# Kernel optimization log

Hardware: AMD Instinct MI355X
Metric: run time of the kernel (lower is better)

The kernel has to match this reference:

```python
import jax, jax.numpy as jnp
import numpy as np
from jax import lax

RSM_K = 35
PFM_K = 31


def _box_sum(x, k):
    # Separable zero-padded box sum, equivalent to conv2d with a uniform kxk
    # kernel and padding=k//2 (odd k -> SAME). x: [B,1,H,W]
    p = k // 2
    pad = ((0, 0), (0, 0), (p, p), (0, 0))
    x = lax.reduce_window(x, 0.0, lax.add, (1, 1, k, 1), (1, 1, 1, 1), pad)
    pad = ((0, 0), (0, 0), (0, 0), (p, p))
    x = lax.reduce_window(x, 0.0, lax.add, (1, 1, 1, k), (1, 1, 1, 1), pad)
    return x


def _dilate(x, k):
    # Separable morphological dilation == max_pool2d(kernel=k, stride=1, pad=k//2).
    # -inf padding matches torch's max_pool2d padding semantics for 0/1 masks.
    p = k // 2
    ninf = -jnp.inf
    pad = ((0, 0), (0, 0), (p, p), (0, 0))
    x = lax.reduce_window(x, ninf, lax.max, (1, 1, k, 1), (1, 1, 1, 1), pad)
    pad = ((0, 0), (0, 0), (0, 0), (p, p))
    x = lax.reduce_window(x, ninf, lax.max, (1, 1, 1, k), (1, 1, 1, 1), pad)
    return x


def setup_inputs() -> dict:
    key = jax.random.key(0)
    # Sparse binary lesion mask, values exactly 0.0 / 1.0, shape [B,1,H,W]
    masks = (jax.random.uniform(key, (32, 1, 768, 768)) < 0.02).astype(jnp.float32)
    return {"masks": masks}


def reference(masks):
    # RSM: probability map = uniform 35x35 box average (conv2d with 1/k^2 kernel)
    rsm = _box_sum(masks, RSM_K) * (1.0 / (RSM_K * RSM_K))  # [B,1,H,W]
    # PFM: 1 = lesion, 0 = surrounding (inside 31x31 dilation), 2 = ignore
    dilated = _dilate(masks, PFM_K)
    pfm = jnp.where(masks > 0.5, 1, jnp.where(dilated > 0.5, 0, 2))
    pfm = pfm.astype(jnp.int32)[:, 0, :, :]  # [B,H,W]
    return rsm, pfm
```

## Files before the change

kernel.cpp:

```cpp
#include <hip/hip_runtime.h>


#define BATCH 32
#define HH 768
#define WW 768
#define NPIX (HH * WW)

constexpr int TYO  = 48;
constexpr int HALO = 17;
constexpr int ROWS = TYO + 2 * HALO;
constexpr int NSEG = 12;
constexpr int SSEG = NSEG + 2;
constexpr int NT   = 768;
constexpr int NG   = 4;
constexpr int RPG  = TYO / NG;
constexpr int CT   = 192;
constexpr int CPT  = 4;

__global__ __launch_bounds__(NT)
void label_gen_fused(const float* __restrict__ in, float* __restrict__ out) {
    __shared__ unsigned long long sbits[ROWS][SSEG];

    const int tid  = threadIdx.x;
    const int lane = tid & 63;
    const int wv   = tid >> 6;
    const int y0   = blockIdx.x * TYO;
    const int b    = blockIdx.y;
    const float* __restrict__ src = in + (size_t)b * NPIX;

    for (int lr = wv; lr < ROWS; lr += 12) {
        const int r = y0 - HALO + lr;
        unsigned long long bb[NSEG];
        if ((unsigned)r < (unsigned)HH) {
            const float* rp = src + (size_t)r * WW;
            #pragma unroll
            for (int j = 0; j < NSEG; ++j)
                bb[j] = __ballot(rp[64 * j + lane] > 0.5f);
        } else {
            #pragma unroll
            for (int j = 0; j < NSEG; ++j) bb[j] = 0ull;
        }
        if (lane == 0) {
            sbits[lr][0] = 0ull;
            #pragma unroll
            for (int j = 0; j < NSEG; ++j) sbits[lr][j + 1] = bb[j];
            sbits[lr][SSEG - 1] = 0ull;
        }
    }
    __syncthreads();

    const int g   = tid / CT;
    const int ct  = tid - g * CT;
    const int c0  = CPT * ct;
    const int yb  = y0 + RPG * g;
    const int lr0 = RPG * g;
    const int s   = c0 - HALO;
    const int q   = (s >> 6) + 1;
    const int sh  = s & 63;

    auto win = [&](int lr) -> unsigned long long {
        return (sbits[lr][q] >> sh) | (sbits[lr][q + 1] << (64 - sh));
    };
    const unsigned long long M35 = (1ull << 35) - 1;
    const unsigned long long M31 = (1ull << 31) - 1;
    auto bit = [](unsigned long long w, int k) -> int { return (int)((w >> k) & 1ull); };

    auto h35swar = [&](unsigned long long w) -> uint2 {
        const int h0 = (int)__popcll(w & M35);
        const int h1 = h0 + bit(w, 35) - bit(w, 0);
        const int h2 = h1 + bit(w, 36) - bit(w, 1);
        const int h3 = h2 + bit(w, 37) - bit(w, 2);
        return make_uint2((unsigned)(h0 | (h1 << 16)), (unsigned)(h2 | (h3 << 16)));
    };
    auto h31swar = [&](unsigned long long w) -> uint2 {
        const int d0 = (int)__popcll((w >> 2) & M31);
        const int d1 = d0 + bit(w, 33) - bit(w, 2);
        const int d2 = d1 + bit(w, 34) - bit(w, 3);
        const int d3 = d2 + bit(w, 35) - bit(w, 4);
        return make_uint2((unsigned)(d0 | (d1 << 16)), (unsigned)(d2 | (d3 << 16)));
    };

    uint2 v35 = make_uint2(0u, 0u), v31 = make_uint2(0u, 0u);
    #pragma unroll
    for (int k = 0; k < 35; ++k) {
        const unsigned long long w = win(lr0 + k);
        const uint2 a = h35swar(w);
        v35.x += a.x; v35.y += a.y;
        if (k >= 2 && k <= 32) {
            const uint2 d = h31swar(w);
            v31.x += d.x; v31.y += d.y;
        }
    }

    float* orow = out + (size_t)b * NPIX + (size_t)yb * WW + c0;
    float* prow = orow + (size_t)BATCH * NPIX;

    for (int i = 0; i < RPG; ++i) {
        const int lr = lr0 + HALO + i;
        const unsigned long long mwin = win(lr);

        float4 r4, p4;
        r4.x = (float)(v35.x & 0xFFFFu) * (1.0f / 1225.0f);
        r4.y = (float)(v35.x >> 16)     * (1.0f / 1225.0f);
        r4.z = (float)(v35.y & 0xFFFFu) * (1.0f / 1225.0f);
        r4.w = (float)(v35.y >> 16)     * (1.0f / 1225.0f);
        p4.x = bit(mwin, 17) ? 1.0f : ((v31.x & 0xFFFFu) ? 0.0f : 2.0f);
        p4.y = bit(mwin, 18) ? 1.0f : ((v31.x >> 16)     ? 0.0f : 2.0f);
        p4.z = bit(mwin, 19) ? 1.0f : ((v31.y & 0xFFFFu) ? 0.0f : 2.0f);
        p4.w = bit(mwin, 20) ? 1.0f : ((v31.y >> 16)     ? 0.0f : 2.0f);

        *(float4*)orow = r4;
        *(float4*)prow = p4;
        orow += WW; prow += WW;

        if (i < RPG - 1) {
            const uint2 e35 = h35swar(win(lr + 18));
            const uint2 l35 = h35swar(win(lr - 17));
            const uint2 e31 = h31swar(win(lr + 16));
            const uint2 l31 = h31swar(win(lr - 15));
            v35.x = v35.x + e35.x - l35.x;  v35.y = v35.y + e35.y - l35.y;
            v31.x = v31.x + e31.x - l31.x;  v31.y = v31.y + e31.y - l31.y;
        }
    }
}

extern "C" void kernel_launch(void* const* d_in, const int* in_sizes, int n_in,
                              void* d_out, int out_size, void* d_ws, size_t ws_size,
                              hipStream_t stream) {
    const float* masks = (const float*)d_in[0];
    float* out = (float*)d_out;
    dim3 grid(HH / TYO, BATCH);
    label_gen_fused<<<grid, NT, 0, stream>>>(masks, out);
}
```

Measured before the change: 213.9 us.

## Precompute per-row packed horizontal sums in LDS to share across vertical windows

```diff
diff --git a/kernel.cpp b/kernel.cpp
--- a/kernel.cpp
+++ b/kernel.cpp
@@ -15,11 +15,11 @@
 constexpr int NG   = 4;
 constexpr int RPG  = TYO / NG;
 constexpr int CT   = 192;
-constexpr int CPT  = 4;
 
 __global__ __launch_bounds__(NT)
 void label_gen_fused(const float* __restrict__ in, float* __restrict__ out) {
     __shared__ unsigned long long sbits[ROWS][SSEG];
+    __shared__ unsigned int hm[ROWS][CT];
 
     const int tid  = threadIdx.x;
     const int lane = tid & 63;
@@ -28,7 +28,7 @@
     const int b    = blockIdx.y;
     const float* __restrict__ src = in + (size_t)b * NPIX;
 
-    for (int lr = wv; lr < ROWS; lr += 12) {
+    for (int lr = wv; lr < ROWS; lr += NT / 64) {
         const int r = y0 - HALO + lr;
         unsigned long long bb[NSEG];
         if ((unsigned)r < (unsigned)HH) {
@@ -49,47 +49,57 @@
     }
     __syncthreads();
 
+    {
+        const int r0 = tid / CT;
+        const int ct = tid - r0 * CT;
+        const int c0 = 4 * ct;
+        const int s  = c0 - HALO;
+        const int q  = (s >> 6) + 1;
+        const int sh = s & 63;
+        const unsigned long long M35 = (1ull << 35) - 1;
+        for (int lr = r0; lr < ROWS; lr += NG) {
+            const unsigned long long w =
+                (sbits[lr][q] >> sh) | (sbits[lr][q + 1] << (64 - sh));
+            const int h0 = (int)__popcll(w & M35);
+            const int h1 = h0 + (int)((w >> 35) & 1) - (int)(w & 1);
+            const int h2 = h1 + (int)((w >> 36) & 1) - (int)((w >> 1) & 1);
+            const int h3 = h2 + (int)((w >> 37) & 1) - (int)((w >> 2) & 1);
+            unsigned long long sm = w | (w >> 1);
+            sm |= sm >> 2; sm |= sm >> 4; sm |= sm >> 8;
+            const unsigned int o4 = (unsigned int)(((sm >> 2) | (sm >> 17)) & 0xFull);
+            const unsigned int m4 = (unsigned int)((w >> 17) & 0xFull);
+            const unsigned int mb =
+                (((m4 & 1u) | ((m4 & 2u) << 7) | ((m4 & 4u) << 14) | ((m4 & 8u) << 21)) << 6);
+            const unsigned int ob =
+                (((o4 & 1u) | ((o4 & 2u) << 7) | ((o4 & 4u) << 14) | ((o4 & 8u) << 21)) << 7);
+            hm[lr][ct] = (unsigned)h0 | ((unsigned)h1 << 8) | ((unsigned)h2 << 16)
+                       | ((unsigned)h3 << 24) | mb | ob;
+        }
+    }
+    __syncthreads();
+
     const int g   = tid / CT;
     const int ct  = tid - g * CT;
-    const int c0  = CPT * ct;
+    const int c0  = 4 * ct;
     const int yb  = y0 + RPG * g;
     const int lr0 = RPG * g;
-    const int s   = c0 - HALO;
-    const int q   = (s >> 6) + 1;
-    const int sh  = s & 63;
 
-    auto win = [&](int lr) -> unsigned long long {
-        return (sbits[lr][q] >> sh) | (sbits[lr][q + 1] << (64 - sh));
-    };
-    const unsigned long long M35 = (1ull << 35) - 1;
-    const unsigned long long M31 = (1ull << 31) - 1;
-    auto bit = [](unsigned long long w, int k) -> int { return (int)((w >> k) & 1ull); };
+    const unsigned int M6 = 0x003F003Fu;
+    const unsigned int M1 = 0x01010101u;
 
-    auto h35swar = [&](unsigned long long w) -> uint2 {
-        const int h0 = (int)__popcll(w & M35);
-        const int h1 = h0 + bit(w, 35) - bit(w, 0);
-        const int h2 = h1 + bit(w, 36) - bit(w, 1);
-        const int h3 = h2 + bit(w, 37) - bit(w, 2);
-        return make_uint2((unsigned)(h0 | (h1 << 16)), (unsigned)(h2 | (h3 << 16)));
-    };
-    auto h31swar = [&](unsigned long long w) -> uint2 {
-        const int d0 = (int)__popcll((w >> 2) & M31);
-        const int d1 = d0 + bit(w, 33) - bit(w, 2);
-        const int d2 = d1 + bit(w, 34) - bit(w, 3);
-        const int d3 = d2 + bit(w, 35) - bit(w, 4);
-        return make_uint2((unsigned)(d0 | (d1 << 16)), (unsigned)(d2 | (d3 << 16)));
-    };
-
-    uint2 v35 = make_uint2(0u, 0u), v31 = make_uint2(0u, 0u);
+    unsigned int vA = 0, vB = 0;
+    unsigned int c31 = 0;
+    unsigned int ring_e[2], ring_l[2];
     #pragma unroll
     for (int k = 0; k < 35; ++k) {
-        const unsigned long long w = win(lr0 + k);
-        const uint2 a = h35swar(w);
-        v35.x += a.x; v35.y += a.y;
-        if (k >= 2 && k <= 32) {
-            const uint2 d = h31swar(w);
-            v31.x += d.x; v31.y += d.y;
-        }
+        const unsigned int x = hm[lr0 + k][ct];
+        vA += x & M6;
+        vB += (x >> 8) & M6;
+        if (k >= 2 && k <= 32) c31 += (x >> 7) & M1;
+        if (k == 0)  ring_l[0] = x;
+        if (k == 1)  ring_l[1] = x;
+        if (k == 33) ring_e[0] = x;
+        if (k == 34) ring_e[1] = x;
     }
 
     float* orow = out + (size_t)b * NPIX + (size_t)yb * WW + c0;
@@ -97,29 +107,32 @@
 
     for (int i = 0; i < RPG; ++i) {
         const int lr = lr0 + HALO + i;
-        const unsigned long long mwin = win(lr);
+        const unsigned int xc = hm[lr][ct];
 
         float4 r4, p4;
-        r4.x = (float)(v35.x & 0xFFFFu) * (1.0f / 1225.0f);
-        r4.y = (float)(v35.x >> 16)     * (1.0f / 1225.0f);
-        r4.z = (float)(v35.y & 0xFFFFu) * (1.0f / 1225.0f);
-        r4.w = (float)(v35.y >> 16)     * (1.0f / 1225.0f);
-        p4.x = bit(mwin, 17) ? 1.0f : ((v31.x & 0xFFFFu) ? 0.0f : 2.0f);
-        p4.y = bit(mwin, 18) ? 1.0f : ((v31.x >> 16)     ? 0.0f : 2.0f);
-        p4.z = bit(mwin, 19) ? 1.0f : ((v31.y & 0xFFFFu) ? 0.0f : 2.0f);
-        p4.w = bit(mwin, 20) ? 1.0f : ((v31.y >> 16)     ? 0.0f : 2.0f);
+        r4.x = (float)(vA & 0xFFFFu) * (1.0f / 1225.0f);
+        r4.y = (float)(vB & 0xFFFFu) * (1.0f / 1225.0f);
+        r4.z = (float)(vA >> 16)     * (1.0f / 1225.0f);
+        r4.w = (float)(vB >> 16)     * (1.0f / 1225.0f);
+        p4.x = ((xc >> 6) & 1u)  ? 1.0f : ((c31 & 0xFFu)         ? 0.0f : 2.0f);
+        p4.y = ((xc >> 14) & 1u) ? 1.0f : (((c31 >> 8) & 0xFFu)  ? 0.0f : 2.0f);
+        p4.z = ((xc >> 22) & 1u) ? 1.0f : (((c31 >> 16) & 0xFFu) ? 0.0f : 2.0f);
+        p4.w = ((xc >> 30) & 1u) ? 1.0f : ((c31 >> 24)           ? 0.0f : 2.0f);
 
         *(float4*)orow = r4;
         *(float4*)prow = p4;
         orow += WW; prow += WW;
 
         if (i < RPG - 1) {
-            const uint2 e35 = h35swar(win(lr + 18));
-            const uint2 l35 = h35swar(win(lr - 17));
-            const uint2 e31 = h31swar(win(lr + 16));
-            const uint2 l31 = h31swar(win(lr - 15));
-            v35.x = v35.x + e35.x - l35.x;  v35.y = v35.y + e35.y - l35.y;
-            v31.x = v31.x + e31.x - l31.x;  v31.y = v31.y + e31.y - l31.y;
+            const unsigned int xe   = hm[lr + 18][ct];
+            const unsigned int xl31 = hm[lr0 + 2 + i][ct];
+            const unsigned int xe31 = ring_e[i & 1];
+            const unsigned int xl   = ring_l[i & 1];
+            ring_e[i & 1] = xe;
+            ring_l[i & 1] = xl31;
+            vA  = (vA + (xe & M6)) - (xl & M6);
+            vB  = (vB + ((xe >> 8) & M6)) - ((xl >> 8) & M6);
+            c31 = (c31 + ((xe31 >> 7) & M1)) - ((xl31 >> 7) & M1);
         }
     }
 }
```

Measured after the change: 211.8 us. Within noise of the previous version (-1.0%).

## Precompute packed horizontal sums into LDS ring and roll vertical window per column

Applied to the files above, without the earlier changes.

```diff
diff --git a/kernel.cpp b/kernel.cpp
--- a/kernel.cpp
+++ b/kernel.cpp
@@ -7,19 +7,19 @@
 #define NPIX (HH * WW)
 
 constexpr int TYO  = 48;
-constexpr int HALO = 17;
-constexpr int ROWS = TYO + 2 * HALO;
 constexpr int NSEG = 12;
 constexpr int SSEG = NSEG + 2;
 constexpr int NT   = 768;
-constexpr int NG   = 4;
-constexpr int RPG  = TYO / NG;
 constexpr int CT   = 192;
-constexpr int CPT  = 4;
+constexpr int PRO  = 34;
+constexpr int RING = 48;
+
+__device__ __forceinline__ int m48(int x) { return (x >= RING) ? x - RING : x; }
 
 __global__ __launch_bounds__(NT)
-void label_gen_fused(const float* __restrict__ in, float* __restrict__ out) {
-    __shared__ unsigned long long sbits[ROWS][SSEG];
+void label_gen_roll(const float* __restrict__ in, float* __restrict__ out) {
+    __shared__ unsigned long long sbits[PRO][SSEG];
+    __shared__ unsigned int hm[RING][CT];
 
     const int tid  = threadIdx.x;
     const int lane = tid & 63;
@@ -28,8 +28,8 @@
     const int b    = blockIdx.y;
     const float* __restrict__ src = in + (size_t)b * NPIX;
 
-    for (int lr = wv; lr < ROWS; lr += 12) {
-        const int r = y0 - HALO + lr;
+    auto packrow = [&](int lr, int slot) {
+        const int r = y0 - 17 + lr;
         unsigned long long bb[NSEG];
         if ((unsigned)r < (unsigned)HH) {
             const float* rp = src + (size_t)r * WW;
@@ -41,85 +41,79 @@
             for (int j = 0; j < NSEG; ++j) bb[j] = 0ull;
         }
         if (lane == 0) {
-            sbits[lr][0] = 0ull;
+            sbits[slot][0] = 0ull;
             #pragma unroll
-            for (int j = 0; j < NSEG; ++j) sbits[lr][j + 1] = bb[j];
-            sbits[lr][SSEG - 1] = 0ull;
+            for (int j = 0; j < NSEG; ++j) sbits[slot][j + 1] = bb[j];
+            sbits[slot][SSEG - 1] = 0ull;
         }
-    }
+    };
+
+    const int gH  = tid / CT;
+    const int ctH = tid - gH * CT;
+    const int sH  = 4 * ctH - 17;
+    const int qH  = (sH >> 6) + 1;
+    const int shH = sH & 63;
+    const unsigned long long M35 = (1ull << 35) - 1;
+    auto bit = [](unsigned long long w, int k) -> unsigned {
+        return (unsigned)((w >> k) & 1ull);
+    };
+    auto hrow = [&](int slot, int ring) {
+        const unsigned long long w =
+            (sbits[slot][qH] >> shH) | (sbits[slot][qH + 1] << (64 - shH));
+        const unsigned h0 = (unsigned)__popcll(w & M35);
+        const unsigned h1 = h0 + bit(w, 35) - bit(w, 0);
+        const unsigned h2 = h1 + bit(w, 36) - bit(w, 1);
+        const unsigned h3 = h2 + bit(w, 37) - bit(w, 2);
+        unsigned long long sm = w | (w >> 1);
+        sm |= sm >> 2; sm |= sm >> 4; sm |= sm >> 8;
+        const unsigned o4 = (unsigned)(((sm >> 2) | (sm >> 17)) & 0xFull);
+        const unsigned m4 = (unsigned)((w >> 17) & 0xFull);
+        hm[ring][ctH] = h0 | (h1 << 8) | (h2 << 16) | (h3 << 24)
+                      | ((m4 & 1u) << 6)  | ((m4 & 2u) << 13)
+                      | ((m4 & 4u) << 20) | ((m4 & 8u) << 27)
+                      | ((o4 & 1u) << 7)  | ((o4 & 2u) << 14)
+                      | ((o4 & 4u) << 21) | ((o4 & 8u) << 28);
+    };
+
+    for (int lr = wv; lr < PRO; lr += 12) packrow(lr, lr);
+    __syncthreads();
+    for (int lr = gH; lr < PRO; lr += 4) hrow(lr, lr);
     __syncthreads();
 
-    const int g   = tid / CT;
-    const int ct  = tid - g * CT;
-    const int c0  = CPT * ct;
-    const int yb  = y0 + RPG * g;
-    const int lr0 = RPG * g;
-    const int s   = c0 - HALO;
-    const int q   = (s >> 6) + 1;
-    const int sh  = s & 63;
-
-    auto win = [&](int lr) -> unsigned long long {
-        return (sbits[lr][q] >> sh) | (sbits[lr][q + 1] << (64 - sh));
-    };
-    const unsigned long long M35 = (1ull << 35) - 1;
-    const unsigned long long M31 = (1ull << 31) - 1;
-    auto bit = [](unsigned long long w, int k) -> int { return (int)((w >> k) & 1ull); };
-
-    auto h35swar = [&](unsigned long long w) -> uint2 {
-        const int h0 = (int)__popcll(w & M35);
-        const int h1 = h0 + bit(w, 35) - bit(w, 0);
-        const int h2 = h1 + bit(w, 36) - bit(w, 1);
-        const int h3 = h2 + bit(w, 37) - bit(w, 2);
-        return make_uint2((unsigned)(h0 | (h1 << 16)), (unsigned)(h2 | (h3 << 16)));
-    };
-    auto h31swar = [&](unsigned long long w) -> uint2 {
-        const int d0 = (int)__popcll((w >> 2) & M31);
-        const int d1 = d0 + bit(w, 33) - bit(w, 2);
-        const int d2 = d1 + bit(w, 34) - bit(w, 3);
-        const int d3 = d2 + bit(w, 35) - bit(w, 4);
-        return make_uint2((unsigned)(d0 | (d1 << 16)), (unsigned)(d2 | (d3 << 16)));
-    };
-
-    uint2 v35 = make_uint2(0u, 0u), v31 = make_uint2(0u, 0u);
+    const int wrd = tid >> 2;
+    const int sh8 = (tid & 3) * 8;
+    int v35 = 0, c31 = 0;
     #pragma unroll
-    for (int k = 0; k < 35; ++k) {
-        const unsigned long long w = win(lr0 + k);
-        const uint2 a = h35swar(w);
-        v35.x += a.x; v35.y += a.y;
-        if (k >= 2 && k <= 32) {
-            const uint2 d = h31swar(w);
-            v31.x += d.x; v31.y += d.y;
-        }
+    for (int k = 0; k < PRO; ++k) {
+        const unsigned x = hm[k][wrd] >> sh8;
+        v35 += (int)(x & 0x3Fu);
+        if (k >= 2 && k <= 32) c31 += (int)((x >> 7) & 1u);
     }
 
-    float* orow = out + (size_t)b * NPIX + (size_t)yb * WW + c0;
+    float* orow = out + (size_t)b * NPIX + (size_t)y0 * WW + tid;
     float* prow = orow + (size_t)BATCH * NPIX;
 
-    for (int i = 0; i < RPG; ++i) {
-        const int lr = lr0 + HALO + i;
-        const unsigned long long mwin = win(lr);
-
-        float4 r4, p4;
-        r4.x = (float)(v35.x & 0xFFFFu) * (1.0f / 1225.0f);
-        r4.y = (float)(v35.x >> 16)     * (1.0f / 1225.0f);
-        r4.z = (float)(v35.y & 0xFFFFu) * (1.0f / 1225.0f);
-        r4.w = (float)(v35.y >> 16)     * (1.0f / 1225.0f);
-        p4.x = bit(mwin, 17) ? 1.0f : ((v31.x & 0xFFFFu) ? 0.0f : 2.0f);
-        p4.y = bit(mwin, 18) ? 1.0f : ((v31.x >> 16)     ? 0.0f : 2.0f);
-        p4.z = bit(mwin, 19) ? 1.0f : ((v31.y & 0xFFFFu) ? 0.0f : 2.0f);
-        p4.w = bit(mwin, 20) ? 1.0f : ((v31.y >> 16)     ? 0.0f : 2.0f);
-
-        *(float4*)orow = r4;
-        *(float4*)prow = p4;
-        orow += WW; prow += WW;
-
-        if (i < RPG - 1) {
-            const uint2 e35 = h35swar(win(lr + 18));
-            const uint2 l35 = h35swar(win(lr - 17));
-            const uint2 e31 = h31swar(win(lr + 16));
-            const uint2 l31 = h31swar(win(lr - 15));
-            v35.x = v35.x + e35.x - l35.x;  v35.y = v35.y + e35.y - l35.y;
-            v31.x = v31.x + e31.x - l31.x;  v31.y = v31.y + e31.y - l31.y;
+    for (int j = 0; j < 4; ++j) {
+        const int base = PRO + 12 * j;
+        packrow(base + wv, wv);
+        __syncthreads();
+        for (int r = gH; r < 12; r += 4) hrow(r, m48(base + r));
+        __syncthreads();
+        for (int ii = 0; ii < 12; ++ii) {
+            const int i = 12 * j + ii;
+            const unsigned xe = hm[m48(i + 34)][wrd] >> sh8;
+            v35 += (int)(xe & 0x3Fu);
+            if (i > 0) {
+                const unsigned xl = hm[m48(i - 1)][wrd] >> sh8;
+                const unsigned xa = hm[m48(i + 32)][wrd] >> sh8;
+                const unsigned xs = hm[m48(i + 1)][wrd] >> sh8;
+                v35 -= (int)(xl & 0x3Fu);
+                c31 += (int)((xa >> 7) & 1u) - (int)((xs >> 7) & 1u);
+            }
+            const unsigned xc = hm[m48(i + 17)][wrd] >> sh8;
+            *orow = (float)v35 * (1.0f / 1225.0f);
+            *prow = ((xc >> 6) & 1u) ? 1.0f : (c31 ? 0.0f : 2.0f);
+            orow += WW; prow += WW;
         }
     }
 }
@@ -130,5 +124,5 @@
     const float* masks = (const float*)d_in[0];
     float* out = (float*)d_out;
     dim3 grid(HH / TYO, BATCH);
-    label_gen_fused<<<grid, NT, 0, stream>>>(masks, out);
+    label_gen_roll<<<grid, NT, 0, stream>>>(masks, out);
 }
```

After: 214.6 us. No clear change (+0.3%).
